# Optimization experiments

Hardware: AMD Instinct MI355X
Metric: run time of the kernel (lower is better)

Reference implementation:

```python
import jax, jax.numpy as jnp
import numpy as np

N_NODES = 100000
N_EDGES = 3200000


def _gcn_conv(x, src, dst, norm_e, W, b, n_nodes):
    # PyG GCNConv: x @ W, propagate with symmetric norm (self-loops already
    # appended to src/dst with their norm coefficients in norm_e), then + b.
    h = x @ W                                    # [N, out]
    msgs = h[src] * norm_e[:, None]              # [E+N, out] gather + scale
    out = jax.ops.segment_sum(msgs, dst, num_segments=n_nodes)
    return out + b


def _prep_graph(edge_index, n_nodes):
    # Add self-loops and compute symmetric GCN normalization coefficients.
    src, dst = edge_index[0], edge_index[1]
    loops = jnp.arange(n_nodes, dtype=src.dtype)
    src = jnp.concatenate([src, loops])
    dst = jnp.concatenate([dst, loops])
    deg = jax.ops.segment_sum(jnp.ones_like(dst, dtype=jnp.float32), dst,
                              num_segments=n_nodes)
    dinv = jnp.where(deg > 0, jax.lax.rsqrt(deg), 0.0)
    norm_e = dinv[src] * dinv[dst]               # [E+N]
    return src, dst, norm_e


def setup_inputs() -> dict:
    key = jax.random.key(0)
    ks = jax.random.split(key, 5)
    k = 11  # max_colors + 1
    X = jax.random.normal(ks[0], (N_NODES, k), dtype=jnp.float32)
    edge_index = jax.random.randint(ks[1], (2, N_EDGES), 0, N_NODES,
                                    dtype=jnp.int64)
    # Glorot-ish scale for the tiny weight matrices.
    W1 = jax.random.normal(ks[2], (k, k), dtype=jnp.float32) * (1.0 / np.sqrt(k))
    W2 = jax.random.normal(ks[3], (k, k), dtype=jnp.float32) * (1.0 / np.sqrt(k))
    W3 = jax.random.normal(ks[4], (k, 10), dtype=jnp.float32) * (1.0 / np.sqrt(k))
    return {
        "X": X, "edge_index": edge_index,
        "W1": W1, "b1": jnp.zeros((k,), jnp.float32),
        "W2": W2, "b2": jnp.zeros((k,), jnp.float32),
        "W3": W3, "b3": jnp.zeros((10,), jnp.float32),
    }


def reference(X, edge_index, W1, b1, W2, b2, W3, b3):
    n_nodes = X.shape[0]
    src, dst, norm_e = _prep_graph(edge_index, n_nodes)
    h = _gcn_conv(X, src, dst, norm_e, W1, b1, n_nodes)
    h = jax.nn.gelu(h)
    h = _gcn_conv(h, src, dst, norm_e, W2, b2, n_nodes)
    h = jax.nn.gelu(h)
    h = _gcn_conv(h, src, dst, norm_e, W3, b3, n_nodes)
    return jax.nn.log_softmax(h, axis=1)
```

## Files before the change

kernel.cpp:

```cpp
#include <hip/hip_runtime.h>
#include <hip/hip_fp16.h>
#include <math.h>

#define N_NODES 100000
#define N_EDGES 3200000

#define NPBC  512
#define NBC   196
#define KB2   512
#define CH2   6250

#define HS    12

__device__ __forceinline__ float gelu_tanh(float x) {
    const float c = 0.7978845608028654f;
    float t = tanhf(c * (x + 0.044715f * x * x * x));
    return 0.5f * x * (1.0f + t);
}

__global__ void detect_kernel(const unsigned int* __restrict__ ei, int* __restrict__ flag) {
    unsigned int v = ei[2 * threadIdx.x + 1];
    unsigned long long m = __ballot(v != 0u);
    if (threadIdx.x == 0) flag[0] = (m != 0ull) ? 1 : 0;
}

__device__ __forceinline__ int load_idx(const void* ei, int f, size_t pos) {
    if (f) return ((const int*)ei)[pos];
    return (int)((const long long*)ei)[pos];
}

__global__ void cnt_kernel(const void* __restrict__ ei, const int* __restrict__ flag,
                           int* __restrict__ bcnt) {
    __shared__ int lcnt[NBC];
    int k = blockIdx.x, t = threadIdx.x;
    for (int b = t; b < NBC; b += 256) lcnt[b] = 0;
    __syncthreads();
    int f = flag[0];
    int lo = k * CH2, hi = min(lo + CH2, N_EDGES);
    for (int e = lo + t; e < hi; e += 256) {
        int d = load_idx(ei, f, (size_t)N_EDGES + e);
        atomicAdd(&lcnt[d >> 9], 1);
    }
    __syncthreads();
    for (int b = t; b < NBC; b += 256) bcnt[b * KB2 + k] = lcnt[b];
}

__global__ void bprefix_kernel(int* __restrict__ bcnt, int* __restrict__ tot) {
    int b = blockIdx.x * blockDim.x + threadIdx.x;
    if (b >= NBC) return;
    int run = 0;
    int base = b * KB2;
    for (int k = 0; k < KB2; k++) {
        int v = bcnt[base + k];
        bcnt[base + k] = run;
        run += v;
    }
    tot[b] = run;
}

__global__ void bscan_kernel(const int* __restrict__ tot, int* __restrict__ bbase,
                             int* __restrict__ off) {
    __shared__ int sh[256];
    int t = threadIdx.x;
    int v = (t < NBC) ? tot[t] : 0;
    sh[t] = v;
    __syncthreads();
    int val = v;
    for (int o = 1; o < 256; o <<= 1) {
        int add = (t >= o) ? sh[t - o] : 0;
        __syncthreads();
        val += add;
        sh[t] = val;
        __syncthreads();
    }
    if (t < NBC) bbase[t] = val - v;
    if (t == NBC - 1) off[N_NODES] = val;
}

__global__ void part2_kernel(const void* __restrict__ ei, const int* __restrict__ flag,
                             const int* __restrict__ boff, const int* __restrict__ bbase,
                             int* __restrict__ btmp) {
    __shared__ int lcnt[NBC];
    __shared__ int lbase[NBC];
    int k = blockIdx.x, t = threadIdx.x;
    for (int b = t; b < NBC; b += 256) {
        lcnt[b] = 0;
        lbase[b] = bbase[b] + boff[b * KB2 + k];
    }
    __syncthreads();
    int f = flag[0];
    int lo = k * CH2, hi = min(lo + CH2, N_EDGES);
    for (int e = lo + t; e < hi; e += 256) {
        int s = load_idx(ei, f, e);
        int d = load_idx(ei, f, (size_t)N_EDGES + e);
        int b = d >> 9;
        int pos = atomicAdd(&lcnt[b], 1);
        btmp[lbase[b] + pos] = s | ((d & (NPBC - 1)) << 17);
    }
}

__global__ void build2_kernel(const int* __restrict__ tot, const int* __restrict__ bbase,
                              const int* __restrict__ btmp, int* __restrict__ csr,
                              int* __restrict__ off, float* __restrict__ dinv) {
    __shared__ int lcnt[NPBC];
    __shared__ int lcur[NPBC];
    __shared__ int ssc[NPBC];
    int b = blockIdx.x;
    int t = threadIdx.x;
    int cnt = tot[b];
    int base = bbase[b];
    lcnt[t] = 0;
    __syncthreads();
    const int* bt = btmp + base;
    for (int i = t; i < cnt; i += NPBC) atomicAdd(&lcnt[bt[i] >> 17], 1);
    __syncthreads();
    int c = lcnt[t];
    ssc[t] = c;
    __syncthreads();
    int val = c;
    for (int o = 1; o < NPBC; o <<= 1) {
        int add = (t >= o) ? ssc[t - o] : 0;
        __syncthreads();
        val += add;
        ssc[t] = val;
        __syncthreads();
    }
    int excl = val - c;
    lcur[t] = excl;
    int node = b * NPBC + t;
    if (node < N_NODES) {
        off[node] = base + excl;
        dinv[node] = rsqrtf((float)c + 1.0f);
    }
    __syncthreads();
    for (int i = t; i < cnt; i += NPBC) {
        int e = bt[i];
        int p = atomicAdd(&lcur[e >> 17], 1);
        csr[base + p] = e & 0x1FFFF;
    }
}

__device__ __forceinline__ void acc_row(const __half* __restrict__ h2, int n, float* a) {
    const __half* r = h2 + (size_t)n * HS;
    uint4 u = *(const uint4*)r;
    uint2 v = *(const uint2*)(r + 8);
    union { unsigned int u; __half2 h; } cv;
    float2 f;
    cv.u = u.x; f = __half22float2(cv.h); a[0] += f.x; a[1] += f.y;
    cv.u = u.y; f = __half22float2(cv.h); a[2] += f.x; a[3] += f.y;
    cv.u = u.z; f = __half22float2(cv.h); a[4] += f.x; a[5] += f.y;
    cv.u = u.w; f = __half22float2(cv.h); a[6] += f.x; a[7] += f.y;
    cv.u = v.x; f = __half22float2(cv.h); a[8] += f.x; a[9] += f.y;
    cv.u = v.y; f = __half22float2(cv.h); a[10] += f.x;
}

__device__ __forceinline__ void gather8(const int* __restrict__ csr, int lo, int hi, int p,
                                        const __half* __restrict__ h2in, float* a) {
    int e = lo + p;
    if (e >= hi) return;
    int s = csr[e];
    for (e += 8; e < hi; e += 8) {
        int s_next = csr[e];
        acc_row(h2in, s, a);
        s = s_next;
    }
    acc_row(h2in, s, a);
}

__global__ void node1_kernel(const float* __restrict__ X, const float* __restrict__ W,
                             const float* __restrict__ dinv, __half* __restrict__ h2) {
    int n = blockIdx.x * blockDim.x + threadIdx.x;
    if (n >= N_NODES) return;
    float x[11];
#pragma unroll
    for (int i = 0; i < 11; i++) x[i] = X[n * 11 + i];
    float di = dinv[n];
#pragma unroll
    for (int j = 0; j < 11; j++) {
        float a = 0.0f;
#pragma unroll
        for (int i = 0; i < 11; i++) a += x[i] * W[i * 11 + j];
        h2[(size_t)n * HS + j] = __float2half(di * a);
    }
    h2[(size_t)n * HS + 11] = __float2half(0.0f);
}

template <int OUT>
__global__ void mid_kernel(const int* __restrict__ off, const int* __restrict__ csr,
                           const __half* __restrict__ h2in, const float* __restrict__ bias,
                           const float* __restrict__ W, const float* __restrict__ dinv,
                           __half* __restrict__ h2out) {
    int tid = blockIdx.x * blockDim.x + threadIdx.x;
    int n = tid >> 3;
    int p = tid & 7;
    if (n >= N_NODES) return;
    int lo = off[n], hi = off[n + 1];
    float a[11];
#pragma unroll
    for (int i = 0; i < 11; i++) a[i] = 0.0f;
    if (p == 0) acc_row(h2in, n, a);
    gather8(csr, lo, hi, p, h2in, a);
#pragma unroll
    for (int i = 0; i < 11; i++) {
        a[i] += __shfl_xor(a[i], 1);
        a[i] += __shfl_xor(a[i], 2);
        a[i] += __shfl_xor(a[i], 4);
    }
    float di = dinv[n];
    float t[11];
#pragma unroll
    for (int i = 0; i < 11; i++) t[i] = gelu_tanh(di * a[i] + bias[i]);
#pragma unroll
    for (int j0 = 0; j0 < 2; j0++) {
        int j = p + 8 * j0;
        if (j >= HS) continue;
        float o = 0.0f;
        if (j < OUT) {
            float acc = 0.0f;
#pragma unroll
            for (int i = 0; i < 11; i++) acc += t[i] * W[i * OUT + j];
            o = di * acc;
        }
        h2out[(size_t)n * HS + j] = __float2half(o);
    }
}

__global__ void final_kernel(const int* __restrict__ off, const int* __restrict__ csr,
                             const __half* __restrict__ h2in, const float* __restrict__ bias,
                             const float* __restrict__ dinv, float* __restrict__ out) {
    int tid = blockIdx.x * blockDim.x + threadIdx.x;
    int n = tid >> 3;
    int p = tid & 7;
    if (n >= N_NODES) return;
    int lo = off[n], hi = off[n + 1];
    float a[11];
#pragma unroll
    for (int i = 0; i < 11; i++) a[i] = 0.0f;
    if (p == 0) acc_row(h2in, n, a);
    gather8(csr, lo, hi, p, h2in, a);
#pragma unroll
    for (int i = 0; i < 10; i++) {
        a[i] += __shfl_xor(a[i], 1);
        a[i] += __shfl_xor(a[i], 2);
        a[i] += __shfl_xor(a[i], 4);
    }
    float di = dinv[n];
    float t[10];
    float m = -1e30f;
#pragma unroll
    for (int j = 0; j < 10; j++) {
        t[j] = di * a[j] + bias[j];
        m = fmaxf(m, t[j]);
    }
    float s = 0.0f;
#pragma unroll
    for (int j = 0; j < 10; j++) s += expf(t[j] - m);
    float ls = logf(s);
    for (int j = p; j < 10; j += 8) out[(size_t)n * 10 + j] = t[j] - m - ls;
}

extern "C" void kernel_launch(void* const* d_in, const int* in_sizes, int n_in,
                              void* d_out, int out_size, void* d_ws, size_t ws_size,
                              hipStream_t stream) {
    const float* X  = (const float*)d_in[0];
    const void*  ei = d_in[1];
    const float* W1 = (const float*)d_in[2];
    const float* b1 = (const float*)d_in[3];
    const float* W2 = (const float*)d_in[4];
    const float* b2 = (const float*)d_in[5];
    const float* W3 = (const float*)d_in[6];
    const float* b3 = (const float*)d_in[7];
    float* out = (float*)d_out;

    const size_t N = N_NODES;
    const size_t E = N_EDGES;
    __half* h2a = (__half*)d_ws;
    __half* h2b = h2a + (size_t)HS * N;
    int*   csr  = (int*)(h2b + (size_t)HS * N);
    int*   btmp = csr + E;
    int*   bcnt = btmp + E;
    int*   tot  = bcnt + (size_t)NBC * KB2;
    int*   bbase= tot + NBC + 4;
    int*   off  = bbase + NBC + 4;
    float* dinv = (float*)(off + N + 4);
    int*   flag = (int*)(dinv + N);

    const int nb = (N_NODES + 255) / 256;
    const int gb8 = (8 * N_NODES + 255) / 256;

    detect_kernel<<<1, 64, 0, stream>>>((const unsigned int*)ei, flag);
    cnt_kernel<<<KB2, 256, 0, stream>>>(ei, flag, bcnt);
    bprefix_kernel<<<(NBC + 63) / 64, 64, 0, stream>>>(bcnt, tot);
    bscan_kernel<<<1, 256, 0, stream>>>(tot, bbase, off);
    part2_kernel<<<KB2, 256, 0, stream>>>(ei, flag, bcnt, bbase, btmp);
    build2_kernel<<<NBC, NPBC, 0, stream>>>(tot, bbase, btmp, csr, off, dinv);

    node1_kernel<<<nb, 256, 0, stream>>>(X, W1, dinv, h2a);
    mid_kernel<11><<<gb8, 256, 0, stream>>>(off, csr, h2a, b1, W2, dinv, h2b);
    mid_kernel<10><<<gb8, 256, 0, stream>>>(off, csr, h2b, b2, W3, dinv, h2a);
    final_kernel<<<gb8, 256, 0, stream>>>(off, csr, h2a, b3, dinv, out);
}
```

Baseline: 163.4 us.

## Parallelize bucket prefix scan with wave shuffles and use smaller buckets

The per-bucket prefix over block counts now uses one 64-lane wave per bucket with shuffle scans, replacing a serial loop of one thread per bucket. The count matrix is transposed to block-major layout. Buckets shrink to 256 nodes, which doubles the bucket count and the number of partition blocks. This lets build2 run 391 blocks of 256 threads, at the cost of more shared-memory counters and a larger count matrix.

```diff
diff --git a/kernel.cpp b/kernel.cpp
--- a/kernel.cpp
+++ b/kernel.cpp
@@ -5,10 +5,10 @@
 #define N_NODES 100000
 #define N_EDGES 3200000
 
-#define NPBC  512
-#define NBC   196
-#define KB2   512
-#define CH2   6250
+#define NPBC  256
+#define NBC   391
+#define KB2   1024
+#define CH2   3125
 
 #define HS    12
 
@@ -39,34 +39,48 @@
     int lo = k * CH2, hi = min(lo + CH2, N_EDGES);
     for (int e = lo + t; e < hi; e += 256) {
         int d = load_idx(ei, f, (size_t)N_EDGES + e);
-        atomicAdd(&lcnt[d >> 9], 1);
-    }
-    __syncthreads();
-    for (int b = t; b < NBC; b += 256) bcnt[b * KB2 + k] = lcnt[b];
+        atomicAdd(&lcnt[d >> 8], 1);
+    }
+    __syncthreads();
+    for (int b = t; b < NBC; b += 256) bcnt[(size_t)k * NBC + b] = lcnt[b];
 }
 
 __global__ void bprefix_kernel(int* __restrict__ bcnt, int* __restrict__ tot) {
-    int b = blockIdx.x * blockDim.x + threadIdx.x;
-    if (b >= NBC) return;
-    int run = 0;
-    int base = b * KB2;
-    for (int k = 0; k < KB2; k++) {
-        int v = bcnt[base + k];
-        bcnt[base + k] = run;
-        run += v;
-    }
-    tot[b] = run;
+    int gid = blockIdx.x * blockDim.x + threadIdx.x;
+    int w = gid >> 6;
+    int l = gid & 63;
+    if (w >= NBC) return;
+    int v[16];
+    int s = 0;
+#pragma unroll
+    for (int i = 0; i < 16; i++) {
+        v[i] = bcnt[(size_t)(l * 16 + i) * NBC + w];
+        s += v[i];
+    }
+    int scan = s;
+#pragma unroll
+    for (int o = 1; o < 64; o <<= 1) {
+        int x = __shfl_up(scan, o);
+        if (l >= o) scan += x;
+    }
+    int run = scan - s;
+#pragma unroll
+    for (int i = 0; i < 16; i++) {
+        bcnt[(size_t)(l * 16 + i) * NBC + w] = run;
+        run += v[i];
+    }
+    if (l == 63) tot[w] = scan;
 }
 
 __global__ void bscan_kernel(const int* __restrict__ tot, int* __restrict__ bbase,
                              int* __restrict__ off) {
-    __shared__ int sh[256];
+    __shared__ int sh[512];
     int t = threadIdx.x;
     int v = (t < NBC) ? tot[t] : 0;
     sh[t] = v;
     __syncthreads();
     int val = v;
-    for (int o = 1; o < 256; o <<= 1) {
+    for (int o = 1; o < 512; o <<= 1) {
         int add = (t >= o) ? sh[t - o] : 0;
         __syncthreads();
         val += add;
@@ -85,7 +99,7 @@
     int k = blockIdx.x, t = threadIdx.x;
     for (int b = t; b < NBC; b += 256) {
         lcnt[b] = 0;
-        lbase[b] = bbase[b] + boff[b * KB2 + k];
+        lbase[b] = bbase[b] + boff[(size_t)k * NBC + b];
     }
     __syncthreads();
     int f = flag[0];
@@ -93,7 +107,7 @@
     for (int e = lo + t; e < hi; e += 256) {
         int s = load_idx(ei, f, e);
         int d = load_idx(ei, f, (size_t)N_EDGES + e);
-        int b = d >> 9;
+        int b = d >> 8;
         int pos = atomicAdd(&lcnt[b], 1);
         btmp[lbase[b] + pos] = s | ((d & (NPBC - 1)) << 17);
     }
@@ -279,7 +293,7 @@
     int*   csr  = (int*)(h2b + (size_t)HS * N);
     int*   btmp = csr + E;
     int*   bcnt = btmp + E;
-    int*   tot  = bcnt + (size_t)NBC * KB2;
+    int*   tot  = bcnt + (size_t)KB2 * NBC;
     int*   bbase= tot + NBC + 4;
     int*   off  = bbase + NBC + 4;
     float* dinv = (float*)(off + N + 4);
@@ -287,11 +301,12 @@
 
     const int nb = (N_NODES + 255) / 256;
     const int gb8 = (8 * N_NODES + 255) / 256;
+    const int pb = (NBC * 64 + 255) / 256;
 
     detect_kernel<<<1, 64, 0, stream>>>((const unsigned int*)ei, flag);
     cnt_kernel<<<KB2, 256, 0, stream>>>(ei, flag, bcnt);
-    bprefix_kernel<<<(NBC + 63) / 64, 64, 0, stream>>>(bcnt, tot);
-    bscan_kernel<<<1, 256, 0, stream>>>(tot, bbase, off);
+    bprefix_kernel<<<pb, 256, 0, stream>>>(bcnt, tot);
+    bscan_kernel<<<1, 512, 0, stream>>>(tot, bbase, off);
     part2_kernel<<<KB2, 256, 0, stream>>>(ei, flag, bcnt, bbase, btmp);
     build2_kernel<<<NBC, NPBC, 0, stream>>>(tot, bbase, btmp, csr, off, dinv);
 
```

New measurement: 165.5 us. No clear change (+1.3%).

## Fuse CSR preprocessing kernels and fold first-layer transform into build

Applied to the files above, without the earlier changes.

Drops the separate detect, bprefix/bscan and node1 launches. The index-width detection moves into the count and partition kernels, the two prefix passes merge into one single-block kernel, and the first-layer X@W1 scaled by dinv is computed inside build2. The bucket-count layout is transposed so the per-bucket scan reads coalesced rows, and the chunk count is halved to 256 so that serial scan is shorter. The goal is less launch overhead and fewer tiny serial kernels, at the cost of fewer, larger blocks in the count and partition passes.

```diff
diff --git a/kernel.cpp b/kernel.cpp
--- a/kernel.cpp
+++ b/kernel.cpp
@@ -7,8 +7,8 @@
 
 #define NPBC  512
 #define NBC   196
-#define KB2   512
-#define CH2   6250
+#define KB2   256
+#define CH2   12500
 
 #define HS    12
 
@@ -18,10 +18,14 @@
     return 0.5f * x * (1.0f + t);
 }
 
-__global__ void detect_kernel(const unsigned int* __restrict__ ei, int* __restrict__ flag) {
-    unsigned int v = ei[2 * threadIdx.x + 1];
-    unsigned long long m = __ballot(v != 0u);
-    if (threadIdx.x == 0) flag[0] = (m != 0ull) ? 1 : 0;
+__device__ __forceinline__ int detect_flag(const void* ei, int t, int* sflag) {
+    if (t < 64) {
+        unsigned int v = ((const unsigned int*)ei)[2 * t + 1];
+        unsigned long long m = __ballot(v != 0u);
+        if (t == 0) *sflag = (m != 0ull) ? 1 : 0;
+    }
+    __syncthreads();
+    return *sflag;
 }
 
 __device__ __forceinline__ int load_idx(const void* ei, int f, size_t pos) {
@@ -29,43 +33,38 @@
     return (int)((const long long*)ei)[pos];
 }
 
-__global__ void cnt_kernel(const void* __restrict__ ei, const int* __restrict__ flag,
-                           int* __restrict__ bcnt) {
+__global__ void cnt_kernel(const void* __restrict__ ei, int* __restrict__ bcnt) {
     __shared__ int lcnt[NBC];
+    __shared__ int sflag;
     int k = blockIdx.x, t = threadIdx.x;
+    int f = detect_flag(ei, t, &sflag);
     for (int b = t; b < NBC; b += 256) lcnt[b] = 0;
     __syncthreads();
-    int f = flag[0];
     int lo = k * CH2, hi = min(lo + CH2, N_EDGES);
     for (int e = lo + t; e < hi; e += 256) {
         int d = load_idx(ei, f, (size_t)N_EDGES + e);
         atomicAdd(&lcnt[d >> 9], 1);
     }
     __syncthreads();
-    for (int b = t; b < NBC; b += 256) bcnt[b * KB2 + k] = lcnt[b];
-}
-
-__global__ void bprefix_kernel(int* __restrict__ bcnt, int* __restrict__ tot) {
-    int b = blockIdx.x * blockDim.x + threadIdx.x;
-    if (b >= NBC) return;
-    int run = 0;
-    int base = b * KB2;
-    for (int k = 0; k < KB2; k++) {
-        int v = bcnt[base + k];
-        bcnt[base + k] = run;
-        run += v;
-    }
-    tot[b] = run;
-}
-
-__global__ void bscan_kernel(const int* __restrict__ tot, int* __restrict__ bbase,
-                             int* __restrict__ off) {
+    for (int b = t; b < NBC; b += 256) bcnt[(size_t)k * NBC + b] = lcnt[b];
+}
+
+__global__ void prefix_kernel(int* __restrict__ bcnt, int* __restrict__ tot,
+                              int* __restrict__ bbase, int* __restrict__ off) {
     __shared__ int sh[256];
     int t = threadIdx.x;
-    int v = (t < NBC) ? tot[t] : 0;
-    sh[t] = v;
-    __syncthreads();
-    int val = v;
+    int run = 0;
+    if (t < NBC) {
+#pragma unroll 4
+        for (int k = 0; k < KB2; k++) {
+            int v = bcnt[(size_t)k * NBC + t];
+            bcnt[(size_t)k * NBC + t] = run;
+            run += v;
+        }
+    }
+    sh[t] = (t < NBC) ? run : 0;
+    __syncthreads();
+    int val = sh[t];
     for (int o = 1; o < 256; o <<= 1) {
         int add = (t >= o) ? sh[t - o] : 0;
         __syncthreads();
@@ -73,22 +72,25 @@
         sh[t] = val;
         __syncthreads();
     }
-    if (t < NBC) bbase[t] = val - v;
-    if (t == NBC - 1) off[N_NODES] = val;
-}
-
-__global__ void part2_kernel(const void* __restrict__ ei, const int* __restrict__ flag,
-                             const int* __restrict__ boff, const int* __restrict__ bbase,
-                             int* __restrict__ btmp) {
+    if (t < NBC) {
+        tot[t] = run;
+        bbase[t] = val - run;
+    }
+    if (t == 0) off[N_NODES] = N_EDGES;
+}
+
+__global__ void part2_kernel(const void* __restrict__ ei, const int* __restrict__ boff,
+                             const int* __restrict__ bbase, int* __restrict__ btmp) {
     __shared__ int lcnt[NBC];
     __shared__ int lbase[NBC];
+    __shared__ int sflag;
     int k = blockIdx.x, t = threadIdx.x;
+    int f = detect_flag(ei, t, &sflag);
     for (int b = t; b < NBC; b += 256) {
         lcnt[b] = 0;
-        lbase[b] = bbase[b] + boff[b * KB2 + k];
-    }
-    __syncthreads();
-    int f = flag[0];
+        lbase[b] = bbase[b] + boff[(size_t)k * NBC + b];
+    }
+    __syncthreads();
     int lo = k * CH2, hi = min(lo + CH2, N_EDGES);
     for (int e = lo + t; e < hi; e += 256) {
         int s = load_idx(ei, f, e);
@@ -101,7 +103,9 @@
 
 __global__ void build2_kernel(const int* __restrict__ tot, const int* __restrict__ bbase,
                               const int* __restrict__ btmp, int* __restrict__ csr,
-                              int* __restrict__ off, float* __restrict__ dinv) {
+                              int* __restrict__ off, float* __restrict__ dinv,
+                              const float* __restrict__ X, const float* __restrict__ W,
+                              __half* __restrict__ h2) {
     __shared__ int lcnt[NPBC];
     __shared__ int lcur[NPBC];
     __shared__ int ssc[NPBC];
@@ -128,15 +132,29 @@
     int excl = val - c;
     lcur[t] = excl;
     int node = b * NPBC + t;
+    float di = rsqrtf((float)c + 1.0f);
     if (node < N_NODES) {
         off[node] = base + excl;
-        dinv[node] = rsqrtf((float)c + 1.0f);
+        dinv[node] = di;
     }
     __syncthreads();
     for (int i = t; i < cnt; i += NPBC) {
         int e = bt[i];
         int p = atomicAdd(&lcur[e >> 17], 1);
         csr[base + p] = e & 0x1FFFF;
+    }
+    if (node < N_NODES) {
+        float x[11];
+#pragma unroll
+        for (int i = 0; i < 11; i++) x[i] = X[(size_t)node * 11 + i];
+#pragma unroll
+        for (int j = 0; j < 11; j++) {
+            float a = 0.0f;
+#pragma unroll
+            for (int i = 0; i < 11; i++) a += x[i] * W[i * 11 + j];
+            h2[(size_t)node * HS + j] = __float2half(di * a);
+        }
+        h2[(size_t)node * HS + 11] = __float2half(0.0f);
     }
 }
 
@@ -167,24 +185,6 @@
     acc_row(h2in, s, a);
 }
 
-__global__ void node1_kernel(const float* __restrict__ X, const float* __restrict__ W,
-                             const float* __restrict__ dinv, __half* __restrict__ h2) {
-    int n = blockIdx.x * blockDim.x + threadIdx.x;
-    if (n >= N_NODES) return;
-    float x[11];
-#pragma unroll
-    for (int i = 0; i < 11; i++) x[i] = X[n * 11 + i];
-    float di = dinv[n];
-#pragma unroll
-    for (int j = 0; j < 11; j++) {
-        float a = 0.0f;
-#pragma unroll
-        for (int i = 0; i < 11; i++) a += x[i] * W[i * 11 + j];
-        h2[(size_t)n * HS + j] = __float2half(di * a);
-    }
-    h2[(size_t)n * HS + 11] = __float2half(0.0f);
-}
-
 template <int OUT>
 __global__ void mid_kernel(const int* __restrict__ off, const int* __restrict__ csr,
                            const __half* __restrict__ h2in, const float* __restrict__ bias,
@@ -279,23 +279,18 @@
     int*   csr  = (int*)(h2b + (size_t)HS * N);
     int*   btmp = csr + E;
     int*   bcnt = btmp + E;
-    int*   tot  = bcnt + (size_t)NBC * KB2;
+    int*   tot  = bcnt + (size_t)KB2 * NBC;
     int*   bbase= tot + NBC + 4;
     int*   off  = bbase + NBC + 4;
     float* dinv = (float*)(off + N + 4);
-    int*   flag = (int*)(dinv + N);
-
-    const int nb = (N_NODES + 255) / 256;
+
     const int gb8 = (8 * N_NODES + 255) / 256;
 
-    detect_kernel<<<1, 64, 0, stream>>>((const unsigned int*)ei, flag);
-    cnt_kernel<<<KB2, 256, 0, stream>>>(ei, flag, bcnt);
-    bprefix_kernel<<<(NBC + 63) / 64, 64, 0, stream>>>(bcnt, tot);
-    bscan_kernel<<<1, 256, 0, stream>>>(tot, bbase, off);
-    part2_kernel<<<KB2, 256, 0, stream>>>(ei, flag, bcnt, bbase, btmp);
-    build2_kernel<<<NBC, NPBC, 0, stream>>>(tot, bbase, btmp, csr, off, dinv);
-
-    node1_kernel<<<nb, 256, 0, stream>>>(X, W1, dinv, h2a);
+    cnt_kernel<<<KB2, 256, 0, stream>>>(ei, bcnt);
+    prefix_kernel<<<1, 256, 0, stream>>>(bcnt, tot, bbase, off);
+    part2_kernel<<<KB2, 256, 0, stream>>>(ei, bcnt, bbase, btmp);
+    build2_kernel<<<NBC, NPBC, 0, stream>>>(tot, bbase, btmp, csr, off, dinv,
+                                            X, W1, h2a);
     mid_kernel<11><<<gb8, 256, 0, stream>>>(off, csr, h2a, b1, W2, dinv, h2b);
     mid_kernel<10><<<gb8, 256, 0, stream>>>(off, csr, h2b, b2, W3, dinv, h2a);
     final_kernel<<<gb8, 256, 0, stream>>>(off, csr, h2a, b3, dinv, out);
```

New measurement: 171.3 us. +4.8%, slower.
